# Kernel tuning notes

Measured on AMD Instinct MI355X. Metric: run time of the kernel, lower is better.

## Reference

```python
import jax, jax.numpy as jnp
import numpy as np
import math

B, H, T, D = 4, 16, 1024, 64
DEPTH = 12
LAMBDA_INIT = 0.8 - 0.6 * math.exp(-0.3 * DEPTH)


def setup_inputs() -> dict:
    key = jax.random.key(0)
    ks = jax.random.split(key, 10)
    return {
        "query_states": jax.random.normal(ks[0], (B, H, T, D), jnp.float32),
        "key_states": jax.random.normal(ks[1], (B, H, T, D), jnp.float32),
        # la_1: feature_map_k applied to query, feature_map_q applied to key (as in source)
        "W1_q": jax.random.normal(ks[2], (H, D, D), jnp.float32),
        "W1_k": jax.random.normal(ks[3], (H, D, D), jnp.float32),
        "W2_q": jax.random.normal(ks[4], (H, D, D), jnp.float32),
        "W2_k": jax.random.normal(ks[5], (H, D, D), jnp.float32),
        "lambda_q1": jax.random.normal(ks[6], (D,), jnp.float32) * 0.1,
        "lambda_k1": jax.random.normal(ks[7], (D,), jnp.float32) * 0.1,
        "lambda_q2": jax.random.normal(ks[8], (D,), jnp.float32) * 0.1,
        "lambda_k2": jax.random.normal(ks[9], (D,), jnp.float32) * 0.1,
    }


def _branch(q, k, Wq, Wk):
    # per-head linear feature maps, then kernelized attention weights
    qf = jnp.einsum('bhld,hde->bhle', q, Wq)
    kf = jnp.einsum('bhld,hde->bhle', k, Wk)
    aw = jnp.einsum('bhld,bhkd->bhlk', qf, kf)  # [B,H,T,T]
    t = q.shape[2]
    mask = jnp.tril(jnp.ones((t, t), dtype=bool), k=1)  # tril(diagonal=1)
    aw = jnp.where(mask, aw, jnp.zeros((), aw.dtype))
    return aw / jnp.sum(aw, axis=-1, keepdims=True)


def reference(query_states, key_states, W1_q, W1_k, W2_q, W2_k,
              lambda_q1, lambda_k1, lambda_q2, lambda_k2):
    lam1 = jnp.exp(jnp.sum(lambda_q1 * lambda_k1))
    lam2 = jnp.exp(jnp.sum(lambda_q2 * lambda_k2))
    lambda_full = (lam1 - lam2 + LAMBDA_INIT).astype(query_states.dtype)
    aw1 = _branch(query_states, key_states, W1_q, W1_k)
    aw2 = _branch(query_states, key_states, W2_q, W2_k)
    return aw1 - lambda_full * aw2
```

## Files before the change

### kernel.cpp

```cpp
#include <hip/hip_runtime.h>

#define Bn 4
#define Hn 16
#define Tn 1024
#define Dn 64
#define N4 (Bn*Hn*Tn*Dn)

__device__ __constant__ float LAMBDA_INIT_F = 0.78360576653162445f;

__global__ void k_lambda(const float* __restrict__ lq1, const float* __restrict__ lk1,
                         const float* __restrict__ lq2, const float* __restrict__ lk2,
                         float* __restrict__ lam_out) {
    int l = threadIdx.x;
    float p1 = lq1[l] * lk1[l];
    float p2 = lq2[l] * lk2[l];
    #pragma unroll
    for (int m = 1; m < 64; m <<= 1) {
        p1 += __shfl_xor(p1, m);
        p2 += __shfl_xor(p2, m);
    }
    if (l == 0) lam_out[0] = expf(p1) - expf(p2) + LAMBDA_INIT_F;
}

__global__ __launch_bounds__(256) void k_proj(const float* __restrict__ src,
                                              const float* __restrict__ W,
                                              float* __restrict__ dst) {
    __shared__ float Qs[64][68];
    __shared__ float Wt[64][68];
    int t  = threadIdx.x;
    int bx = blockIdx.x;
    int bh = bx >> 4;
    int r0 = (bx & 15) * 64;
    int h  = bh & (Hn - 1);

    const float* sbase = src + (size_t)bh * Tn * Dn + (size_t)r0 * Dn;
    const float* wbase = W + (size_t)h * Dn * Dn;

    #pragma unroll
    for (int it = 0; it < 4; ++it) {
        int f4 = it * 256 + t;
        int r  = f4 >> 4;
        int d0 = (f4 & 15) << 2;
        float4 v = *(const float4*)&sbase[(size_t)r * Dn + d0];
        *(float4*)&Qs[r][d0] = v;
        float4 w = *(const float4*)&wbase[(size_t)r * Dn + d0];
        Wt[d0 + 0][r] = w.x; Wt[d0 + 1][r] = w.y;
        Wt[d0 + 2][r] = w.z; Wt[d0 + 3][r] = w.w;
    }
    __syncthreads();

    int tx = t & 15, ty = t >> 4;
    float acc[4][4];
    #pragma unroll
    for (int i = 0; i < 4; ++i)
        #pragma unroll
        for (int j = 0; j < 4; ++j) acc[i][j] = 0.f;

    #pragma unroll
    for (int d0 = 0; d0 < 64; d0 += 4) {
        float qa[4][4], wb[4][4];
        #pragma unroll
        for (int i = 0; i < 4; ++i) {
            float4 v = *(const float4*)&Qs[4 * ty + i][d0];
            qa[i][0] = v.x; qa[i][1] = v.y; qa[i][2] = v.z; qa[i][3] = v.w;
        }
        #pragma unroll
        for (int j = 0; j < 4; ++j) {
            float4 v = *(const float4*)&Wt[4 * tx + j][d0];
            wb[j][0] = v.x; wb[j][1] = v.y; wb[j][2] = v.z; wb[j][3] = v.w;
        }
        #pragma unroll
        for (int i = 0; i < 4; ++i)
            #pragma unroll
            for (int j = 0; j < 4; ++j)
                #pragma unroll
                for (int p = 0; p < 4; ++p)
                    acc[i][j] = fmaf(qa[i][p], wb[j][p], acc[i][j]);
    }

    float* dbase = dst + (size_t)bh * Tn * Dn + (size_t)r0 * Dn;
    #pragma unroll
    for (int i = 0; i < 4; ++i) {
        float4 o = make_float4(acc[i][0], acc[i][1], acc[i][2], acc[i][3]);
        *(float4*)&dbase[(size_t)(4 * ty + i) * Dn + 4 * tx] = o;
    }
}

__global__ void k_blocksum(const float* __restrict__ kf1, const float* __restrict__ kf2,
                           float* __restrict__ bs) {
    __shared__ float red[4][64];
    int t  = threadIdx.x;
    int bx = blockIdx.x;
    int j  = bx & 7;
    int br = (bx >> 3) & 1;
    int bh = bx >> 4;
    const float* kf = (br ? kf2 : kf1) + (size_t)bh * Tn * Dn + (size_t)j * 128 * Dn;
    int d = t & 63, rg = t >> 6;
    float p = 0.f;
    #pragma unroll 4
    for (int r = 0; r < 32; ++r) p += kf[(size_t)(rg * 32 + r) * Dn + d];
    red[rg][d] = p;
    __syncthreads();
    if (rg == 0)
        bs[(((size_t)bh * 2 + br) * 8 + j) * 64 + d] =
            red[0][d] + red[1][d] + red[2][d] + red[3][d];
}

__global__ void k_prefix(const float* __restrict__ bs, float* __restrict__ kc) {
    int bx = blockIdx.x;
    int br = bx & 1, bh = bx >> 1;
    int d = threadIdx.x;
    float run = 0.f;
    for (int j = 0; j < 8; ++j) {
        size_t idx = (((size_t)bh * 2 + br) * 8 + j) * 64 + d;
        kc[idx] = run;
        run += bs[idx];
    }
}

__global__ __launch_bounds__(256) void k_s(
    const float* __restrict__ qf1, const float* __restrict__ kf1,
    const float* __restrict__ qf2, const float* __restrict__ kf2,
    const float* __restrict__ kc,  float* __restrict__ inv_out) {
    int bx = blockIdx.x;
    int half = bx & 1, br = (bx >> 1) & 1, bh = bx >> 2;
    int g = threadIdx.x >> 6, d = threadIdx.x & 63;
    int j = half * 4 + g;
    const float* qf = (br ? qf2 : qf1) + (size_t)bh * Tn * Dn;
    const float* kf = (br ? kf2 : kf1) + (size_t)bh * Tn * Dn;
    float run = kc[(((size_t)bh * 2 + br) * 8 + j) * 64 + d];
    int R0 = j * 128;
    float* inv = inv_out + ((size_t)bh * 2 + br) * Tn;

    #pragma unroll 4
    for (int step = 0; step <= 128; ++step) {
        int r = R0 + step;
        if (r < Tn) run += kf[(size_t)r * Dn + d];
        if (step >= 1) {
            int rr = r - 1;
            float dv = qf[(size_t)rr * Dn + d] * run;
            #pragma unroll
            for (int m = 1; m < 64; m <<= 1) dv += __shfl_xor(dv, m);
            if (d == 0) inv[rr] = 1.0f / dv;
        }
    }
}

__global__ __launch_bounds__(256, 4) void k_tile(
    const float* __restrict__ qf1, const float* __restrict__ kf1,
    const float* __restrict__ qf2, const float* __restrict__ kf2,
    const float* __restrict__ inv_g, const float* __restrict__ lamp,
    float* __restrict__ out) {

    __shared__ float As[16][132];
    __shared__ float Bs[16][192];
    __shared__ float scl[2][128];
    __shared__ float e_sh[2];

    int t  = threadIdx.x;
    int vid = (blockIdx.x & 7) * 512 + (blockIdx.x >> 3);
    int bh = vid >> 6;
    int tile = vid & 63;
    int rt = tile >> 3, c = tile & 7;
    int r0 = rt * 128, cb = c * 128;
    int tx = t & 15, ty = t >> 4;

    const float lam = lamp[0];
    const float* qg0 = qf1 + (size_t)bh * Tn * Dn;
    const float* qg1 = qf2 + (size_t)bh * Tn * Dn;
    const float* kg0 = kf1 + (size_t)bh * Tn * Dn;
    const float* kg1 = kf2 + (size_t)bh * Tn * Dn;

    if (c > rt) {
        float ev = 0.f;
        if (c == rt + 1) {
            if (t < 128) {
                int br = t >> 6, d = t & 63;
                const float* qp = br ? qg1 : qg0;
                const float* kp = br ? kg1 : kg0;
                float p = qp[(size_t)(r0 + 127) * Dn + d] * kp[(size_t)cb * Dn + d];
                #pragma unroll
                for (int m = 1; m < 64; m <<= 1) p += __shfl_xor(p, m);
                if (d == 0) e_sh[br] = p;
            }
            __syncthreads();
            float i1 = inv_g[((size_t)bh * 2 + 0) * Tn + r0 + 127];
            float i2 = inv_g[((size_t)bh * 2 + 1) * Tn + r0 + 127];
            ev = e_sh[0] * i1 - lam * (e_sh[1] * i2);
        }
        float4 z = make_float4(0.f, 0.f, 0.f, 0.f);
        #pragma unroll
        for (int i = 0; i < 8; ++i) {
            size_t base = ((size_t)bh * Tn + r0 + 8 * ty + i) * Tn + cb + 8 * tx;
            float4 o0 = z;
            if (ty == 15 && i == 7 && tx == 0) o0.x = ev;
            *(float4*)&out[base] = o0;
            *(float4*)&out[base + 4] = z;
        }
        return;
    }

    {
        int br = t >> 7, row = t & 127;
        float iv = inv_g[((size_t)bh * 2 + br) * Tn + r0 + row];
        scl[br][row] = br ? (-lam * iv) : iv;
    }

    float acc[8][8];
    #pragma unroll
    for (int i = 0; i < 8; ++i)
        #pragma unroll
        for (int j = 0; j < 8; ++j) acc[i][j] = 0.f;

    int rc  = t & 127;
    int kl  = (t >> 7) << 3;
    int rcs = rc + ((rc >> 3) << 2);

    for (int ks = 0; ks < 8; ++ks) {
        const float* qsrc = (ks < 4) ? qg0 : qg1;
        const float* ksrc = (ks < 4) ? kg0 : kg1;
        int kbeg = ((ks & 3) << 4) + kl;
        __syncthreads();
        {
            float s = scl[ks >> 2][rc];
            const float* qrow = &qsrc[(size_t)(r0 + rc) * Dn + kbeg];
            float4 a0 = *(const float4*)qrow;
            float4 a1 = *(const float4*)(qrow + 4);
            As[kl + 0][rc] = a0.x * s; As[kl + 1][rc] = a0.y * s;
            As[kl + 2][rc] = a0.z * s; As[kl + 3][rc] = a0.w * s;
            As[kl + 4][rc] = a1.x * s; As[kl + 5][rc] = a1.y * s;
            As[kl + 6][rc] = a1.z * s; As[kl + 7][rc] = a1.w * s;
            const float* krow = &ksrc[(size_t)(cb + rc) * Dn + kbeg];
            float4 b0 = *(const float4*)krow;
            float4 b1 = *(const float4*)(krow + 4);
            Bs[kl + 0][rcs] = b0.x; Bs[kl + 1][rcs] = b0.y;
            Bs[kl + 2][rcs] = b0.z; Bs[kl + 3][rcs] = b0.w;
            Bs[kl + 4][rcs] = b1.x; Bs[kl + 5][rcs] = b1.y;
            Bs[kl + 6][rcs] = b1.z; Bs[kl + 7][rcs] = b1.w;
        }
        __syncthreads();
        int txs = 12 * tx;
        #pragma unroll
        for (int kk = 0; kk < 16; ++kk) {
            float av[8], bv[8];
            float4 v;
            v = *(const float4*)&As[kk][8 * ty];     av[0]=v.x; av[1]=v.y; av[2]=v.z; av[3]=v.w;
            v = *(const float4*)&As[kk][8 * ty + 4]; av[4]=v.x; av[5]=v.y; av[6]=v.z; av[7]=v.w;
            v = *(const float4*)&Bs[kk][txs];        bv[0]=v.x; bv[1]=v.y; bv[2]=v.z; bv[3]=v.w;
            v = *(const float4*)&Bs[kk][txs + 4];    bv[4]=v.x; bv[5]=v.y; bv[6]=v.z; bv[7]=v.w;
            #pragma unroll
            for (int i = 0; i < 8; ++i)
                #pragma unroll
                for (int j = 0; j < 8; ++j)
                    acc[i][j] = fmaf(av[i], bv[j], acc[i][j]);
        }
    }

    if (c == rt) {
        #pragma unroll
        for (int i = 0; i < 8; ++i)
            #pragma unroll
            for (int j = 0; j < 8; ++j)
                if (8 * tx + j > 8 * ty + i + 1) acc[i][j] = 0.f;
    }

    #pragma unroll
    for (int i = 0; i < 8; ++i) {
        float4 o0 = make_float4(acc[i][0], acc[i][1], acc[i][2], acc[i][3]);
        float4 o1 = make_float4(acc[i][4], acc[i][5], acc[i][6], acc[i][7]);
        size_t base = ((size_t)bh * Tn + r0 + 8 * ty + i) * Tn + cb + 8 * tx;
        *(float4*)&out[base] = o0;
        *(float4*)&out[base + 4] = o1;
    }
}

extern "C" void kernel_launch(void* const* d_in, const int* in_sizes, int n_in,
                              void* d_out, int out_size, void* d_ws, size_t ws_size,
                              hipStream_t stream) {
    const float* q   = (const float*)d_in[0];
    const float* k   = (const float*)d_in[1];
    const float* W1q = (const float*)d_in[2];
    const float* W1k = (const float*)d_in[3];
    const float* W2q = (const float*)d_in[4];
    const float* W2k = (const float*)d_in[5];
    const float* lq1 = (const float*)d_in[6];
    const float* lk1 = (const float*)d_in[7];
    const float* lq2 = (const float*)d_in[8];
    const float* lk2 = (const float*)d_in[9];
    float* out = (float*)d_out;
    float* ws  = (float*)d_ws;

    float* qf1 = ws;
    float* kf1 = ws + (size_t)N4;
    float* qf2 = ws + 2 * (size_t)N4;
    float* kf2 = ws + 3 * (size_t)N4;
    float* bs  = ws + 4 * (size_t)N4;
    float* kc  = bs + 65536;
    float* lamp = kc + 65536;
    float* inv_s = lamp + 64;

    k_lambda<<<1, 64, 0, stream>>>(lq1, lk1, lq2, lk2, lamp);
    k_proj<<<1024, 256, 0, stream>>>(q, W1q, qf1);
    k_proj<<<1024, 256, 0, stream>>>(k, W1k, kf1);
    k_proj<<<1024, 256, 0, stream>>>(q, W2q, qf2);
    k_proj<<<1024, 256, 0, stream>>>(k, W2k, kf2);
    k_blocksum<<<1024, 256, 0, stream>>>(kf1, kf2, bs);
    k_prefix<<<128, 64, 0, stream>>>(bs, kc);
    k_s<<<256, 256, 0, stream>>>(qf1, kf1, qf2, kf2, kc, inv_s);
    k_tile<<<4096, 256, 0, stream>>>(qf1, kf1, qf2, kf2, inv_s, lamp, out);
}
```

Baseline: 602.6 us.

## Use split-bf16 MFMA for attention tiles, fuse projections, parallelize normalizer scan

The main tile kernel moves from FP32 FMA to bf16 MFMA. Each feature vector is split into a high and a low bf16 part (three products per pair) to keep near-FP32 accuracy, and the normalization and lambda combination happen in the epilogue. The four projection launches become one kernel that also writes the hi/lo bf16 copies. The per-row normalizer scan now stages keys in LDS and runs with more blocks. The extra bf16 stores and per-element scalar output writes add memory traffic, and accuracy depends on the split-bf16 approximation.

```diff
diff --git a/kernel.cpp b/kernel.cpp
--- a/kernel.cpp
+++ b/kernel.cpp
@@ -5,8 +5,21 @@
 #define Tn 1024
 #define Dn 64
 #define N4 (Bn*Hn*Tn*Dn)
+#define TD (Tn*Dn)
+
+typedef __attribute__((ext_vector_type(8))) short bf16x8;
+typedef __attribute__((ext_vector_type(4))) float f32x4;
 
 __device__ __constant__ float LAMBDA_INIT_F = 0.78360576653162445f;
+
+__device__ inline unsigned short bf16_rne(float x) {
+    unsigned u = __float_as_uint(x);
+    unsigned r = (u + 0x7FFFu + ((u >> 16) & 1u)) >> 16;
+    return (unsigned short)r;
+}
+__device__ inline float bf16_to_f(unsigned short h) {
+    return __uint_as_float(((unsigned)h) << 16);
+}
 
 __global__ void k_lambda(const float* __restrict__ lq1, const float* __restrict__ lk1,
                          const float* __restrict__ lq2, const float* __restrict__ lk2,
@@ -22,18 +35,35 @@
     if (l == 0) lam_out[0] = expf(p1) - expf(p2) + LAMBDA_INIT_F;
 }
 
-__global__ __launch_bounds__(256) void k_proj(const float* __restrict__ src,
-                                              const float* __restrict__ W,
-                                              float* __restrict__ dst) {
+__global__ __launch_bounds__(256) void k_proj4(
+    const float* __restrict__ q, const float* __restrict__ k,
+    const float* __restrict__ W1q, const float* __restrict__ W1k,
+    const float* __restrict__ W2q, const float* __restrict__ W2k,
+    float* __restrict__ qf1, float* __restrict__ kf1,
+    float* __restrict__ qf2, float* __restrict__ kf2,
+    unsigned short* __restrict__ qh1, unsigned short* __restrict__ ql1,
+    unsigned short* __restrict__ kh1, unsigned short* __restrict__ kl1,
+    unsigned short* __restrict__ qh2, unsigned short* __restrict__ ql2,
+    unsigned short* __restrict__ kh2, unsigned short* __restrict__ kl2) {
+
     __shared__ float Qs[64][68];
     __shared__ float Wt[64][68];
+
     int t  = threadIdx.x;
     int bx = blockIdx.x;
-    int bh = bx >> 4;
-    int r0 = (bx & 15) * 64;
+    int idx  = bx & 3;
+    int tile = bx >> 2;
+    int bh = tile >> 4;
+    int r0 = (tile & 15) * 64;
     int h  = bh & (Hn - 1);
 
-    const float* sbase = src + (size_t)bh * Tn * Dn + (size_t)r0 * Dn;
+    const float* src = (idx & 1) ? k : q;
+    const float* W = (idx == 0) ? W1q : (idx == 1) ? W1k : (idx == 2) ? W2q : W2k;
+    float* dst = (idx == 0) ? qf1 : (idx == 1) ? kf1 : (idx == 2) ? qf2 : kf2;
+    unsigned short* dsth = (idx == 0) ? qh1 : (idx == 1) ? kh1 : (idx == 2) ? qh2 : kh2;
+    unsigned short* dstl = (idx == 0) ? ql1 : (idx == 1) ? kl1 : (idx == 2) ? ql2 : kl2;
+
+    const float* sbase = src + (size_t)bh * TD + (size_t)r0 * Dn;
     const float* wbase = W + (size_t)h * Dn * Dn;
 
     #pragma unroll
@@ -78,11 +108,21 @@
                     acc[i][j] = fmaf(qa[i][p], wb[j][p], acc[i][j]);
     }
 
-    float* dbase = dst + (size_t)bh * Tn * Dn + (size_t)r0 * Dn;
+    float* dbase = dst + (size_t)bh * TD + (size_t)r0 * Dn;
+    unsigned short* hbase = dsth + (size_t)bh * TD + (size_t)r0 * Dn;
+    unsigned short* lbase = dstl + (size_t)bh * TD + (size_t)r0 * Dn;
     #pragma unroll
     for (int i = 0; i < 4; ++i) {
+        size_t off = (size_t)(4 * ty + i) * Dn + 4 * tx;
         float4 o = make_float4(acc[i][0], acc[i][1], acc[i][2], acc[i][3]);
-        *(float4*)&dbase[(size_t)(4 * ty + i) * Dn + 4 * tx] = o;
+        *(float4*)&dbase[off] = o;
+        ushort4 hv, lv;
+        hv.x = bf16_rne(o.x); lv.x = bf16_rne(o.x - bf16_to_f(hv.x));
+        hv.y = bf16_rne(o.y); lv.y = bf16_rne(o.y - bf16_to_f(hv.y));
+        hv.z = bf16_rne(o.z); lv.z = bf16_rne(o.z - bf16_to_f(hv.z));
+        hv.w = bf16_rne(o.w); lv.w = bf16_rne(o.w - bf16_to_f(hv.w));
+        *(ushort4*)&hbase[off] = hv;
+        *(ushort4*)&lbase[off] = lv;
     }
 }
 
@@ -94,7 +134,7 @@
     int j  = bx & 7;
     int br = (bx >> 3) & 1;
     int bh = bx >> 4;
-    const float* kf = (br ? kf2 : kf1) + (size_t)bh * Tn * Dn + (size_t)j * 128 * Dn;
+    const float* kf = (br ? kf2 : kf1) + (size_t)bh * TD + (size_t)j * 128 * Dn;
     int d = t & 63, rg = t >> 6;
     float p = 0.f;
     #pragma unroll 4
@@ -118,43 +158,76 @@
     }
 }
 
-__global__ __launch_bounds__(256) void k_s(
+__global__ __launch_bounds__(256) void k_s2(
     const float* __restrict__ qf1, const float* __restrict__ kf1,
     const float* __restrict__ qf2, const float* __restrict__ kf2,
     const float* __restrict__ kc,  float* __restrict__ inv_out) {
+
+    __shared__ float kfl[128][64];
+    __shared__ float wsum[4][64];
+
     int bx = blockIdx.x;
-    int half = bx & 1, br = (bx >> 1) & 1, bh = bx >> 2;
-    int g = threadIdx.x >> 6, d = threadIdx.x & 63;
-    int j = half * 4 + g;
-    const float* qf = (br ? qf2 : qf1) + (size_t)bh * Tn * Dn;
-    const float* kf = (br ? kf2 : kf1) + (size_t)bh * Tn * Dn;
+    int j = bx & 7, br = (bx >> 3) & 1, bh = bx >> 4;
+    int t = threadIdx.x;
+    int g = t >> 6, d = t & 63;
+    int R0 = j * 128;
+
+    const float* qf = (br ? qf2 : qf1) + (size_t)bh * TD;
+    const float* kf = (br ? kf2 : kf1) + (size_t)bh * TD;
+
+    #pragma unroll
+    for (int it = 0; it < 8; ++it) {
+        int f4 = it * 256 + t;
+        int r = f4 >> 4, c4 = (f4 & 15) << 2;
+        *(float4*)&kfl[r][c4] = *(const float4*)&kf[(size_t)(R0 + r) * Dn + c4];
+    }
+    __syncthreads();
+
+    float ps = 0.f;
+    #pragma unroll 8
+    for (int r = 0; r < 32; ++r) ps += kfl[g * 32 + r][d];
+    wsum[g][d] = ps;
+    __syncthreads();
+
     float run = kc[(((size_t)bh * 2 + br) * 8 + j) * 64 + d];
-    int R0 = j * 128;
+    #pragma unroll
+    for (int g2 = 0; g2 < 3; ++g2) if (g2 < g) run += wsum[g2][d];
+
     float* inv = inv_out + ((size_t)bh * 2 + br) * Tn;
 
     #pragma unroll 4
-    for (int step = 0; step <= 128; ++step) {
-        int r = R0 + step;
-        if (r < Tn) run += kf[(size_t)r * Dn + d];
-        if (step >= 1) {
-            int rr = r - 1;
+    for (int s = 0; s < 32; ++s) {
+        int a = g * 32 + s;
+        run += kfl[a][d];
+        int rr = R0 + a - 1;
+        if (rr >= 0) {
             float dv = qf[(size_t)rr * Dn + d] * run;
             #pragma unroll
             for (int m = 1; m < 64; m <<= 1) dv += __shfl_xor(dv, m);
             if (d == 0) inv[rr] = 1.0f / dv;
         }
     }
-}
-
-__global__ __launch_bounds__(256, 4) void k_tile(
-    const float* __restrict__ qf1, const float* __restrict__ kf1,
-    const float* __restrict__ qf2, const float* __restrict__ kf2,
+    if (j == 7 && g == 3) {
+        float dv = qf[(size_t)1023 * Dn + d] * run;
+        #pragma unroll
+        for (int m = 1; m < 64; m <<= 1) dv += __shfl_xor(dv, m);
+        if (d == 0) inv[1023] = 1.0f / dv;
+    }
+}
+
+__global__ __launch_bounds__(512, 4) void k_tile(
+    const unsigned short* __restrict__ qh1, const unsigned short* __restrict__ ql1,
+    const unsigned short* __restrict__ qh2, const unsigned short* __restrict__ ql2,
+    const unsigned short* __restrict__ kh1, const unsigned short* __restrict__ kl1,
+    const unsigned short* __restrict__ kh2, const unsigned short* __restrict__ kl2,
+    const float* __restrict__ qf1, const float* __restrict__ qf2,
+    const float* __restrict__ kf1, const float* __restrict__ kf2,
     const float* __restrict__ inv_g, const float* __restrict__ lamp,
     float* __restrict__ out) {
 
-    __shared__ float As[16][132];
-    __shared__ float Bs[16][192];
-    __shared__ float scl[2][128];
+    __shared__ unsigned short Bhs[128 * 40];
+    __shared__ unsigned short Bls[128 * 40];
+    __shared__ float inv_lds[2][128];
     __shared__ float e_sh[2];
 
     int t  = threadIdx.x;
@@ -163,21 +236,17 @@
     int tile = vid & 63;
     int rt = tile >> 3, c = tile & 7;
     int r0 = rt * 128, cb = c * 128;
-    int tx = t & 15, ty = t >> 4;
 
     const float lam = lamp[0];
-    const float* qg0 = qf1 + (size_t)bh * Tn * Dn;
-    const float* qg1 = qf2 + (size_t)bh * Tn * Dn;
-    const float* kg0 = kf1 + (size_t)bh * Tn * Dn;
-    const float* kg1 = kf2 + (size_t)bh * Tn * Dn;
+    const size_t bb = (size_t)bh * TD;
 
     if (c > rt) {
         float ev = 0.f;
         if (c == rt + 1) {
             if (t < 128) {
                 int br = t >> 6, d = t & 63;
-                const float* qp = br ? qg1 : qg0;
-                const float* kp = br ? kg1 : kg0;
+                const float* qp = (br ? qf2 : qf1) + bb;
+                const float* kp = (br ? kf2 : kf1) + bb;
                 float p = qp[(size_t)(r0 + 127) * Dn + d] * kp[(size_t)cb * Dn + d];
                 #pragma unroll
                 for (int m = 1; m < 64; m <<= 1) p += __shfl_xor(p, m);
@@ -191,86 +260,94 @@
         float4 z = make_float4(0.f, 0.f, 0.f, 0.f);
         #pragma unroll
         for (int i = 0; i < 8; ++i) {
-            size_t base = ((size_t)bh * Tn + r0 + 8 * ty + i) * Tn + cb + 8 * tx;
-            float4 o0 = z;
-            if (ty == 15 && i == 7 && tx == 0) o0.x = ev;
-            *(float4*)&out[base] = o0;
-            *(float4*)&out[base + 4] = z;
+            int f = i * 512 + t;
+            int row = f >> 5, c4 = (f & 31) << 2;
+            float4 o = z;
+            if (c == rt + 1 && f == 4064) o.x = ev;
+            *(float4*)&out[((size_t)bh * Tn + r0 + row) * Tn + cb + c4] = o;
         }
         return;
     }
 
-    {
+    if (t < 256) {
         int br = t >> 7, row = t & 127;
-        float iv = inv_g[((size_t)bh * 2 + br) * Tn + r0 + row];
-        scl[br][row] = br ? (-lam * iv) : iv;
-    }
-
-    float acc[8][8];
-    #pragma unroll
-    for (int i = 0; i < 8; ++i)
-        #pragma unroll
-        for (int j = 0; j < 8; ++j) acc[i][j] = 0.f;
-
-    int rc  = t & 127;
-    int kl  = (t >> 7) << 3;
-    int rcs = rc + ((rc >> 3) << 2);
-
-    for (int ks = 0; ks < 8; ++ks) {
-        const float* qsrc = (ks < 4) ? qg0 : qg1;
-        const float* ksrc = (ks < 4) ? kg0 : kg1;
-        int kbeg = ((ks & 3) << 4) + kl;
+        inv_lds[br][row] = inv_g[((size_t)bh * 2 + br) * Tn + r0 + row];
+    }
+
+    int w = t >> 6, l = t & 63;
+    int wr = (w & 3) * 32;
+    int wc = (w >> 2) * 64;
+    int lrow = l & 15, lk = l >> 4;
+
+    f32x4 acc[2][2][4];
+    #pragma unroll
+    for (int b = 0; b < 2; ++b)
+        #pragma unroll
+        for (int rf = 0; rf < 2; ++rf)
+            #pragma unroll
+            for (int cf = 0; cf < 4; ++cf)
+                acc[b][rf][cf] = (f32x4){0.f, 0.f, 0.f, 0.f};
+
+    const unsigned short* qh[2] = { qh1 + bb, qh2 + bb };
+    const unsigned short* ql[2] = { ql1 + bb, ql2 + bb };
+    const unsigned short* khp[2] = { kh1 + bb, kh2 + bb };
+    const unsigned short* klp[2] = { kl1 + bb, kl2 + bb };
+
+    int sc = t & 127;
+    int sg = (t >> 7) & 1;
+    int sq = t >> 8;
+
+    #pragma unroll
+    for (int pass = 0; pass < 4; ++pass) {
+        const int b = pass >> 1, s = pass & 1;
         __syncthreads();
         {
-            float s = scl[ks >> 2][rc];
-            const float* qrow = &qsrc[(size_t)(r0 + rc) * Dn + kbeg];
-            float4 a0 = *(const float4*)qrow;
-            float4 a1 = *(const float4*)(qrow + 4);
-            As[kl + 0][rc] = a0.x * s; As[kl + 1][rc] = a0.y * s;
-            As[kl + 2][rc] = a0.z * s; As[kl + 3][rc] = a0.w * s;
-            As[kl + 4][rc] = a1.x * s; As[kl + 5][rc] = a1.y * s;
-            As[kl + 6][rc] = a1.z * s; As[kl + 7][rc] = a1.w * s;
-            const float* krow = &ksrc[(size_t)(cb + rc) * Dn + kbeg];
-            float4 b0 = *(const float4*)krow;
-            float4 b1 = *(const float4*)(krow + 4);
-            Bs[kl + 0][rcs] = b0.x; Bs[kl + 1][rcs] = b0.y;
-            Bs[kl + 2][rcs] = b0.z; Bs[kl + 3][rcs] = b0.w;
-            Bs[kl + 4][rcs] = b1.x; Bs[kl + 5][rcs] = b1.y;
-            Bs[kl + 6][rcs] = b1.z; Bs[kl + 7][rcs] = b1.w;
+            const unsigned short* srcp =
+                (sg ? klp[b] : khp[b]) + (size_t)(cb + sc) * Dn + s * 32 + sq * 16;
+            bf16x8 v0 = *(const bf16x8*)srcp;
+            bf16x8 v1 = *(const bf16x8*)(srcp + 8);
+            unsigned short* dstp = (sg ? Bls : Bhs) + sc * 40 + sq * 16;
+            *(bf16x8*)dstp = v0;
+            *(bf16x8*)(dstp + 8) = v1;
         }
         __syncthreads();
-        int txs = 12 * tx;
-        #pragma unroll
-        for (int kk = 0; kk < 16; ++kk) {
-            float av[8], bv[8];
-            float4 v;
-            v = *(const float4*)&As[kk][8 * ty];     av[0]=v.x; av[1]=v.y; av[2]=v.z; av[3]=v.w;
-            v = *(const float4*)&As[kk][8 * ty + 4]; av[4]=v.x; av[5]=v.y; av[6]=v.z; av[7]=v.w;
-            v = *(const float4*)&Bs[kk][txs];        bv[0]=v.x; bv[1]=v.y; bv[2]=v.z; bv[3]=v.w;
-            v = *(const float4*)&Bs[kk][txs + 4];    bv[4]=v.x; bv[5]=v.y; bv[6]=v.z; bv[7]=v.w;
+        const unsigned short* aqh = qh[b] + (size_t)(r0 + wr + lrow) * Dn + s * 32 + lk * 8;
+        const unsigned short* aql = ql[b] + (size_t)(r0 + wr + lrow) * Dn + s * 32 + lk * 8;
+        bf16x8 ah0 = *(const bf16x8*)aqh;
+        bf16x8 ah1 = *(const bf16x8*)(aqh + 16 * Dn);
+        bf16x8 al0 = *(const bf16x8*)aql;
+        bf16x8 al1 = *(const bf16x8*)(aql + 16 * Dn);
+        #pragma unroll
+        for (int cf = 0; cf < 4; ++cf) {
+            int col = wc + cf * 16 + lrow;
+            bf16x8 bhf = *(const bf16x8*)&Bhs[col * 40 + lk * 8];
+            bf16x8 blf = *(const bf16x8*)&Bls[col * 40 + lk * 8];
+            acc[b][0][cf] = __builtin_amdgcn_mfma_f32_16x16x32_bf16(ah0, bhf, acc[b][0][cf], 0, 0, 0);
+            acc[b][0][cf] = __builtin_amdgcn_mfma_f32_16x16x32_bf16(ah0, blf, acc[b][0][cf], 0, 0, 0);
+            acc[b][0][cf] = __builtin_amdgcn_mfma_f32_16x16x32_bf16(al0, bhf, acc[b][0][cf], 0, 0, 0);
+            acc[b][1][cf] = __builtin_amdgcn_mfma_f32_16x16x32_bf16(ah1, bhf, acc[b][1][cf], 0, 0, 0);
+            acc[b][1][cf] = __builtin_amdgcn_mfma_f32_16x16x32_bf16(ah1, blf, acc[b][1][cf], 0, 0, 0);
+            acc[b][1][cf] = __builtin_amdgcn_mfma_f32_16x16x32_bf16(al1, bhf, acc[b][1][cf], 0, 0, 0);
+        }
+    }
+
+    #pragma unroll
+    for (int rf = 0; rf < 2; ++rf) {
+        int rowb = wr + rf * 16 + lk * 4;
+        #pragma unroll
+        for (int cf = 0; cf < 4; ++cf) {
+            int col = cb + wc + cf * 16 + lrow;
             #pragma unroll
-            for (int i = 0; i < 8; ++i)
-                #pragma unroll
-                for (int j = 0; j < 8; ++j)
-                    acc[i][j] = fmaf(av[i], bv[j], acc[i][j]);
-        }
-    }
-
-    if (c == rt) {
-        #pragma unroll
-        for (int i = 0; i < 8; ++i)
-            #pragma unroll
-            for (int j = 0; j < 8; ++j)
-                if (8 * tx + j > 8 * ty + i + 1) acc[i][j] = 0.f;
-    }
-
-    #pragma unroll
-    for (int i = 0; i < 8; ++i) {
-        float4 o0 = make_float4(acc[i][0], acc[i][1], acc[i][2], acc[i][3]);
-        float4 o1 = make_float4(acc[i][4], acc[i][5], acc[i][6], acc[i][7]);
-        size_t base = ((size_t)bh * Tn + r0 + 8 * ty + i) * Tn + cb + 8 * tx;
-        *(float4*)&out[base] = o0;
-        *(float4*)&out[base + 4] = o1;
+            for (int rg = 0; rg < 4; ++rg) {
+                int lr = rowb + rg;
+                int grow = r0 + lr;
+                float v1 = acc[0][rf][cf][rg];
+                float v2 = acc[1][rf][cf][rg];
+                if (c == rt && col > grow + 1) { v1 = 0.f; v2 = 0.f; }
+                float o = v1 * inv_lds[0][lr] - lam * (v2 * inv_lds[1][lr]);
+                out[((size_t)bh * Tn + grow) * Tn + col] = o;
+            }
+        }
     }
 }
 
@@ -294,18 +371,27 @@
     float* kf1 = ws + (size_t)N4;
     float* qf2 = ws + 2 * (size_t)N4;
     float* kf2 = ws + 3 * (size_t)N4;
-    float* bs  = ws + 4 * (size_t)N4;
+    unsigned short* us = (unsigned short*)(ws + 4 * (size_t)N4);
+    unsigned short* qh1 = us;
+    unsigned short* ql1 = us + 1 * (size_t)N4;
+    unsigned short* kh1 = us + 2 * (size_t)N4;
+    unsigned short* kl1 = us + 3 * (size_t)N4;
+    unsigned short* qh2 = us + 4 * (size_t)N4;
+    unsigned short* ql2 = us + 5 * (size_t)N4;
+    unsigned short* kh2 = us + 6 * (size_t)N4;
+    unsigned short* kl2 = us + 7 * (size_t)N4;
+    float* bs  = ws + 8 * (size_t)N4;
     float* kc  = bs + 65536;
     float* lamp = kc + 65536;
     float* inv_s = lamp + 64;
 
     k_lambda<<<1, 64, 0, stream>>>(lq1, lk1, lq2, lk2, lamp);
-    k_proj<<<1024, 256, 0, stream>>>(q, W1q, qf1);
-    k_proj<<<1024, 256, 0, stream>>>(k, W1k, kf1);
-    k_proj<<<1024, 256, 0, stream>>>(q, W2q, qf2);
-    k_proj<<<1024, 256, 0, stream>>>(k, W2k, kf2);
+    k_proj4<<<4096, 256, 0, stream>>>(q, k, W1q, W1k, W2q, W2k,
+                                      qf1, kf1, qf2, kf2,
+                                      qh1, ql1, kh1, kl1, qh2, ql2, kh2, kl2);
     k_blocksum<<<1024, 256, 0, stream>>>(kf1, kf2, bs);
     k_prefix<<<128, 64, 0, stream>>>(bs, kc);
-    k_s<<<256, 256, 0, stream>>>(qf1, kf1, qf2, kf2, kc, inv_s);
-    k_tile<<<4096, 256, 0, stream>>>(qf1, kf1, qf2, kf2, inv_s, lamp, out);
-}
+    k_s2<<<1024, 256, 0, stream>>>(qf1, kf1, qf2, kf2, kc, inv_s);
+    k_tile<<<4096, 512, 0, stream>>>(qh1, ql1, qh2, ql2, kh1, kl1, kh2, kl2,
+                                     qf1, qf2, kf1, kf2, inv_s, lamp, out);
+}
```

New measurement: 491.0 us. -18.5%, faster.
